# Kernel tuning notes

Hardware: AMD Instinct MI355X
Metric: run time of the kernel (lower is better)

The kernel has to match this reference:

```python
import jax, jax.numpy as jnp
import numpy as np

NUM_TAGS = 48
START = 46
STOP = 47
B = 1024
S = 512
NEG_INF = -10000.0


def setup_inputs() -> dict:
    key = jax.random.key(0)
    k1, k2, k3, k4 = jax.random.split(key, 4)
    emissions = jax.random.normal(k1, (B, S, NUM_TAGS), dtype=jnp.float32)
    tags = jax.random.randint(k2, (B, S), 0, 46, dtype=jnp.int32)
    lengths = jax.random.randint(k3, (B,), S // 2, S + 1, dtype=jnp.int32)
    mask = (jnp.arange(S, dtype=jnp.int32)[None, :] < lengths[:, None]).astype(jnp.int32)
    # transitions parameter: uniform(-0.1, 0.1), then constraints from reset_parameters
    transitions = jax.random.uniform(k4, (NUM_TAGS, NUM_TAGS), dtype=jnp.float32,
                                     minval=-0.1, maxval=0.1)
    transitions = transitions.at[:, START].set(NEG_INF).at[STOP, :].set(NEG_INF)
    return {"emissions": emissions, "tags": tags, "mask": mask, "transitions": transitions}


def _log_sum_exp(x, axis):
    # matches torch helper: max + log(clamp(sum(exp(x - max)), 1e-10))
    m = jnp.max(x, axis=axis, keepdims=True)
    s = jnp.sum(jnp.exp(x - m), axis=axis, keepdims=True)
    return jnp.squeeze(m + jnp.log(jnp.clip(s, 1e-10)), axis=axis)


def _forward_alg(emissions, transitions, mask):
    b, s, t = emissions.shape
    alpha0 = jnp.full((b, t), NEG_INF, dtype=emissions.dtype).at[:, START].set(0.0)

    def step(alpha, xs):
        emit, m = xs  # emit: (B, T), m: (B,)
        # (B, prev, next)
        nxt = alpha[:, :, None] + transitions[None, :, :] + emit[:, None, :]
        alpha_t = _log_sum_exp(nxt, axis=1)
        alpha = jnp.where(m[:, None] > 0, alpha_t, alpha)
        return alpha, None

    alpha, _ = jax.lax.scan(step, alpha0,
                            (jnp.transpose(emissions, (1, 0, 2)), mask.T))
    terminal = alpha + transitions[STOP][None, :]
    return _log_sum_exp(terminal, axis=1)  # (B,)


def _score_sequence(emissions, transitions, tags, mask):
    b, s, _ = emissions.shape
    start_col = jnp.full((b, 1), START, dtype=tags.dtype)
    tws = jnp.concatenate([start_col, tags], axis=1)  # (B, S+1)
    # transitions[next, prev] per the original _score_sequence
    trans_sc = transitions[tws[:, 1:], tws[:, :-1]]  # (B, S)
    emit_sc = jnp.take_along_axis(emissions, tags[:, :, None].astype(jnp.int32), axis=2)[..., 0]
    score = jnp.sum((trans_sc + emit_sc) * mask.astype(emissions.dtype), axis=1)
    lengths = jnp.sum(mask, axis=1)
    last_tags = jnp.take_along_axis(tags, (lengths - 1)[:, None], axis=1)[:, 0]
    return score + transitions[STOP, last_tags]


def reference(emissions, tags, mask, transitions):
    log_z = _forward_alg(emissions, transitions, mask)
    gold = _score_sequence(emissions, transitions, tags, mask)
    return jnp.mean(log_z - gold)
```

## Files before the change

kernel.cpp:

```cpp
#include <hip/hip_runtime.h>
#include <hip/hip_bf16.h>
#include <stdint.h>
#include <math.h>

#define SLEN 512
#define NT 48
#define TAG_START 46
#define TAG_STOP 47

typedef __attribute__((ext_vector_type(8))) short bf16x8;
typedef __attribute__((ext_vector_type(4))) float f32x4;

typedef const uint32_t __attribute__((address_space(1)))* gptr_t;
typedef uint32_t __attribute__((address_space(3)))* lptr_t;

__device__ __forceinline__ float bcastf(float v, int l) {
  return __int_as_float(__builtin_amdgcn_readlane(__float_as_int(v), l));
}
__device__ __forceinline__ void gload16(const float* g, float* l) {
  __builtin_amdgcn_global_load_lds((gptr_t)(uintptr_t)g, (lptr_t)(uintptr_t)l,
                                   16, 0, 0);
}
__device__ __forceinline__ uint32_t pk2(float a, float b) {
  float2 f;
  f.x = a;
  f.y = b;
  __hip_bfloat162 bb = __float22bfloat162_rn(f);
  uint32_t u;
  __builtin_memcpy(&u, &bb, 4);
  return u;
}

__global__ __launch_bounds__(64) void crf_fwd_kernel(
    const float* __restrict__ em, const int* __restrict__ tags,
    const int* __restrict__ mask, const float* __restrict__ Tr,
    float* __restrict__ ws) {
  const int b = blockIdx.x;
  const int lane = threadIdx.x;
  const int g = lane >> 4;
  const int n = lane & 15;
  __shared__ __align__(16) float lem[2][64 * NT];

  const int* mrow = mask + (size_t)b * SLEN;
  int lc = 0;
  for (int t = lane; t < SLEN; t += 64) lc += mrow[t];
#pragma unroll
  for (int d = 32; d >= 1; d >>= 1) lc += __shfl_xor(lc, d);
  const int len = lc;

  bf16x8 A[3][2];
#pragma unroll
  for (int t = 0; t < 3; ++t) {
#pragma unroll
    for (int c = 0; c < 2; ++c) {
      union { uint32_t u[4]; bf16x8 v; } tmp;
#pragma unroll
      for (int ep = 0; ep < 4; ++ep) {
        float fe[2];
#pragma unroll
        for (int h = 0; h < 2; ++h) {
          const int e = 2 * ep + h;
          const int kl = (e < 4) ? (4 * g + e) : (16 + 4 * g + (e - 4));
          const int ig = 32 * c + kl;
          fe[h] = (ig < NT) ? __expf(Tr[ig * NT + 16 * t + n]) : 0.0f;
        }
        tmp.u[ep] = pk2(fe[0], fe[1]);
      }
      A[t][c] = tmp.v;
    }
  }

  f32x4 v0 = {0.f, 0.f, 0.f, 0.f}, v1 = v0, v2 = v0;
  if (lane == 48) v2.z = 1.0f;
  int cbits = 0;

  const float* embase = em + (size_t)b * SLEN * NT;

  auto dostep = [&](const float* xb) {
    union { uint32_t u[4]; bf16x8 v; } B0, B1;
    B0.u[0] = pk2(v0.x, v0.y);
    B0.u[1] = pk2(v0.z, v0.w);
    B0.u[2] = pk2(v1.x, v1.y);
    B0.u[3] = pk2(v1.z, v1.w);
    B1.u[0] = pk2(v2.x, v2.y);
    B1.u[1] = pk2(v2.z, v2.w);
    B1.u[2] = 0u;
    B1.u[3] = 0u;
    const f32x4 z4 = {0.f, 0.f, 0.f, 0.f};
    f32x4 a0 = __builtin_amdgcn_mfma_f32_16x16x32_bf16(A[0][0], B0.v, z4, 0, 0, 0);
    f32x4 a1 = __builtin_amdgcn_mfma_f32_16x16x32_bf16(A[1][0], B0.v, z4, 0, 0, 0);
    f32x4 a2 = __builtin_amdgcn_mfma_f32_16x16x32_bf16(A[2][0], B0.v, z4, 0, 0, 0);
    a0 = __builtin_amdgcn_mfma_f32_16x16x32_bf16(A[0][1], B1.v, a0, 0, 0, 0);
    a1 = __builtin_amdgcn_mfma_f32_16x16x32_bf16(A[1][1], B1.v, a1, 0, 0, 0);
    a2 = __builtin_amdgcn_mfma_f32_16x16x32_bf16(A[2][1], B1.v, a2, 0, 0, 0);
    const f32x4 x0 = *(const f32x4*)(xb + 4 * g);
    const f32x4 x1 = *(const f32x4*)(xb + 16 + 4 * g);
    const f32x4 x2 = *(const f32x4*)(xb + 32 + 4 * g);
    v0 = a0 * x0;
    v1 = a1 * x1;
    v2 = a2 * x2;
  };

  auto renorm = [&]() {
    f32x4 m4 = __builtin_elementwise_max(__builtin_elementwise_max(v0, v1), v2);
    float m = fmaxf(fmaxf(m4.x, m4.y), fmaxf(m4.z, fmaxf(m4.w, 1e-30f)));
    m = fmaxf(fmaxf(bcastf(m, 0), bcastf(m, 16)),
              fmaxf(bcastf(m, 32), bcastf(m, 48)));
    int ex;
    (void)frexpf(m, &ex);
    const float sc = ldexpf(1.0f, -ex);
    v0 *= sc;
    v1 *= sc;
    v2 *= sc;
    cbits += ex;
  };

  const int nchunks = (len + 63) >> 6;
#pragma unroll
  for (int k = 0; k < 12; ++k)
    gload16(embase + k * 256 + lane * 4, &lem[0][k * 256]);

  for (int c = 0; c < nchunks; ++c) {
    asm volatile("s_waitcnt vmcnt(0)" ::: "memory");
    if (c + 1 < nchunks) {
      const float* src = embase + (size_t)(c + 1) * 64 * NT;
#pragma unroll
      for (int k = 0; k < 12; ++k)
        gload16(src + k * 256 + lane * 4, &lem[(c + 1) & 1][k * 256]);
    }
    float* bufm = lem[c & 1];
    {
      float* row = bufm + lane * NT;
#pragma unroll
      for (int r = 0; r < 12; ++r) {
        f32x4 vx = *(f32x4*)(row + 4 * r);
        vx.x = __expf(vx.x);
        vx.y = __expf(vx.y);
        vx.z = __expf(vx.z);
        vx.w = __expf(vx.w);
        *(f32x4*)(row + 4 * r) = vx;
      }
    }
    const int tend = (len - c * 64 < 64) ? (len - c * 64) : 64;
    int tt = 0;
    for (; tt + 8 <= tend; tt += 8) {
#pragma unroll
      for (int u2 = 0; u2 < 8; ++u2) dostep(bufm + (tt + u2) * NT);
      renorm();
    }
    for (; tt < tend; ++tt) dostep(bufm + tt * NT);
    renorm();
  }

  renorm();
  float zsum = (v0.x + v0.y + v0.z + v0.w) + (v1.x + v1.y + v1.z + v1.w) +
               (v2.x + v2.y + v2.z + v2.w);
#pragma unroll
  for (int d = 32; d >= 1; d >>= 1) zsum += __shfl_xor(zsum, d);
  const float logZ =
      __logf(zsum) + (float)cbits * 0.69314718055994531f + Tr[TAG_STOP * NT];

  const int* trow = tags + (size_t)b * SLEN;
  float gsc = 0.f;
  for (int t = lane; t < len; t += 64) {
    const int tag = trow[t];
    const int prev = (t == 0) ? TAG_START : trow[t - 1];
    gsc += Tr[tag * NT + prev] + embase[(size_t)t * NT + tag];
  }
#pragma unroll
  for (int d = 32; d >= 1; d >>= 1) gsc += __shfl_xor(gsc, d);

  if (lane == 0) {
    const int last = trow[len - 1];
    ws[b] = logZ - (gsc + Tr[TAG_STOP * NT + last]);
  }
}

__global__ void crf_reduce_kernel(const float* __restrict__ ws,
                                  float* __restrict__ out, int n) {
  const int tid = threadIdx.x;
  float v = (tid < n) ? ws[tid] : 0.f;
#pragma unroll
  for (int d = 32; d >= 1; d >>= 1) v += __shfl_xor(v, d);
  __shared__ float part[16];
  if ((tid & 63) == 0) part[tid >> 6] = v;
  __syncthreads();
  if (tid == 0) {
    float s = 0.f;
    for (int i = 0; i < 16; ++i) s += part[i];
    out[0] = s / (float)n;
  }
}

extern "C" void kernel_launch(void* const* d_in, const int* in_sizes, int n_in,
                              void* d_out, int out_size, void* d_ws, size_t ws_size,
                              hipStream_t stream) {
  const float* em = (const float*)d_in[0];
  const int* tags = (const int*)d_in[1];
  const int* mask = (const int*)d_in[2];
  const float* Tr = (const float*)d_in[3];
  const int B = in_sizes[0] / (SLEN * NT);

  float* ws = (float*)d_ws;
  crf_fwd_kernel<<<B, 64, 0, stream>>>(em, tags, mask, Tr, ws);
  crf_reduce_kernel<<<1, 1024, 0, stream>>>(ws, (float*)d_out, B);
}
```

Baseline: 97.33 us.

## Split CRF forward recursion into forward and backward halves meeting in the middle

Each sequence's linear-domain forward algorithm is split into a forward pass over the first half and a backward pass, using the transposed transition matrix, over the second half. Each block now handles two sequences in the two MFMA columns for one direction. A new combine kernel takes the dot product of the saved alpha and beta vectors to get logZ. This halves the serial dependency chain per block while keeping the same block count. It adds an extra kernel launch and workspace round-trip, and it also replaces the bf16 rounding pack with truncation and the renormalisation with cheaper bit tricks.

```diff
diff --git a/kernel.cpp b/kernel.cpp
--- a/kernel.cpp
+++ b/kernel.cpp
@@ -8,45 +8,63 @@
 #define TAG_START 46
 #define TAG_STOP 47
 
+#define WS_QF 0
+#define WS_WB 65536
+#define WS_OUT 131072
+
 typedef __attribute__((ext_vector_type(8))) short bf16x8;
 typedef __attribute__((ext_vector_type(4))) float f32x4;
 
 typedef const uint32_t __attribute__((address_space(1)))* gptr_t;
 typedef uint32_t __attribute__((address_space(3)))* lptr_t;
 
-__device__ __forceinline__ float bcastf(float v, int l) {
-  return __int_as_float(__builtin_amdgcn_readlane(__float_as_int(v), l));
-}
 __device__ __forceinline__ void gload16(const float* g, float* l) {
   __builtin_amdgcn_global_load_lds((gptr_t)(uintptr_t)g, (lptr_t)(uintptr_t)l,
                                    16, 0, 0);
 }
 __device__ __forceinline__ uint32_t pk2(float a, float b) {
-  float2 f;
-  f.x = a;
-  f.y = b;
-  __hip_bfloat162 bb = __float22bfloat162_rn(f);
-  uint32_t u;
-  __builtin_memcpy(&u, &bb, 4);
-  return u;
-}
-
-__global__ __launch_bounds__(64) void crf_fwd_kernel(
+  return __builtin_amdgcn_perm(__float_as_uint(b), __float_as_uint(a),
+                               0x07060302u);
+}
+__device__ __forceinline__ float fmax4(f32x4 v) {
+  return fmaxf(fmaxf(v.x, v.y), fmaxf(v.z, v.w));
+}
+
+__global__ __launch_bounds__(64) void crf_split2_kernel(
     const float* __restrict__ em, const int* __restrict__ tags,
     const int* __restrict__ mask, const float* __restrict__ Tr,
     float* __restrict__ ws) {
-  const int b = blockIdx.x;
+  const int bid = blockIdx.x;
+  const int dir = bid & 1;
+  const int p = bid >> 1;
+  const int b0 = 2 * p, b1 = 2 * p + 1;
   const int lane = threadIdx.x;
   const int g = lane >> 4;
   const int n = lane & 15;
-  __shared__ __align__(16) float lem[2][64 * NT];
-
-  const int* mrow = mask + (size_t)b * SLEN;
-  int lc = 0;
-  for (int t = lane; t < SLEN; t += 64) lc += mrow[t];
-#pragma unroll
-  for (int d = 32; d >= 1; d >>= 1) lc += __shfl_xor(lc, d);
-  const int len = lc;
+  __shared__ __align__(16) float sbuf[2][2][32 * NT];
+
+  int len0, len1;
+  {
+    int lc0 = 0, lc1 = 0;
+    const int* r0 = mask + (size_t)b0 * SLEN;
+    const int* r1 = mask + (size_t)b1 * SLEN;
+    for (int t = lane; t < SLEN; t += 64) {
+      lc0 += r0[t];
+      lc1 += r1[t];
+    }
+#pragma unroll
+    for (int d = 32; d >= 1; d >>= 1) {
+      lc0 += __shfl_xor(lc0, d);
+      lc1 += __shfl_xor(lc1, d);
+    }
+    len0 = lc0;
+    len1 = lc1;
+  }
+  const int m0 = len0 >> 1, m1 = len1 >> 1;
+  const int st0 = dir ? (len0 - m0) : m0;
+  const int st1 = dir ? (len1 - m1) : m1;
+  const int smax = (st0 > st1) ? st0 : st1;
+  const int my_st = (n == 0) ? st0 : ((n == 1) ? st1 : 0);
 
   bf16x8 A[3][2];
 #pragma unroll
@@ -62,7 +80,10 @@
           const int e = 2 * ep + h;
           const int kl = (e < 4) ? (4 * g + e) : (16 + 4 * g + (e - 4));
           const int ig = 32 * c + kl;
-          fe[h] = (ig < NT) ? __expf(Tr[ig * NT + 16 * t + n]) : 0.0f;
+          fe[h] = 0.0f;
+          if (ig < NT)
+            fe[h] = dir ? __expf(Tr[(16 * t + n) * NT + ig])
+                        : __expf(Tr[ig * NT + 16 * t + n]);
         }
         tmp.u[ep] = pk2(fe[0], fe[1]);
       }
@@ -70,116 +91,185 @@
     }
   }
 
-  f32x4 v0 = {0.f, 0.f, 0.f, 0.f}, v1 = v0, v2 = v0;
-  if (lane == 48) v2.z = 1.0f;
+  const f32x4 z4 = {0.f, 0.f, 0.f, 0.f};
+  f32x4 v0 = z4, v1 = z4, v2 = z4;
+  if (dir == 0) {
+    if (n < 2 && g == 3) v2.z = 1.0f;
+  } else {
+    if (n < 2) {
+      const f32x4 one4 = {1.f, 1.f, 1.f, 1.f};
+      v0 = one4;
+      v1 = one4;
+      v2 = one4;
+    }
+  }
   int cbits = 0;
-
-  const float* embase = em + (size_t)b * SLEN * NT;
-
-  auto dostep = [&](const float* xb) {
-    union { uint32_t u[4]; bf16x8 v; } B0, B1;
-    B0.u[0] = pk2(v0.x, v0.y);
-    B0.u[1] = pk2(v0.z, v0.w);
-    B0.u[2] = pk2(v1.x, v1.y);
-    B0.u[3] = pk2(v1.z, v1.w);
-    B1.u[0] = pk2(v2.x, v2.y);
-    B1.u[1] = pk2(v2.z, v2.w);
-    B1.u[2] = 0u;
-    B1.u[3] = 0u;
-    const f32x4 z4 = {0.f, 0.f, 0.f, 0.f};
-    f32x4 a0 = __builtin_amdgcn_mfma_f32_16x16x32_bf16(A[0][0], B0.v, z4, 0, 0, 0);
-    f32x4 a1 = __builtin_amdgcn_mfma_f32_16x16x32_bf16(A[1][0], B0.v, z4, 0, 0, 0);
-    f32x4 a2 = __builtin_amdgcn_mfma_f32_16x16x32_bf16(A[2][0], B0.v, z4, 0, 0, 0);
-    a0 = __builtin_amdgcn_mfma_f32_16x16x32_bf16(A[0][1], B1.v, a0, 0, 0, 0);
-    a1 = __builtin_amdgcn_mfma_f32_16x16x32_bf16(A[1][1], B1.v, a1, 0, 0, 0);
-    a2 = __builtin_amdgcn_mfma_f32_16x16x32_bf16(A[2][1], B1.v, a2, 0, 0, 0);
-    const f32x4 x0 = *(const f32x4*)(xb + 4 * g);
-    const f32x4 x1 = *(const f32x4*)(xb + 16 + 4 * g);
-    const f32x4 x2 = *(const f32x4*)(xb + 32 + 4 * g);
-    v0 = a0 * x0;
-    v1 = a1 * x1;
-    v2 = a2 * x2;
-  };
-
-  auto renorm = [&]() {
-    f32x4 m4 = __builtin_elementwise_max(__builtin_elementwise_max(v0, v1), v2);
-    float m = fmaxf(fmaxf(m4.x, m4.y), fmaxf(m4.z, fmaxf(m4.w, 1e-30f)));
-    m = fmaxf(fmaxf(bcastf(m, 0), bcastf(m, 16)),
-              fmaxf(bcastf(m, 32), bcastf(m, 48)));
-    int ex;
-    (void)frexpf(m, &ex);
-    const float sc = ldexpf(1.0f, -ex);
-    v0 *= sc;
-    v1 *= sc;
-    v2 *= sc;
-    cbits += ex;
-  };
-
-  const int nchunks = (len + 63) >> 6;
-#pragma unroll
-  for (int k = 0; k < 12; ++k)
-    gload16(embase + k * 256 + lane * 4, &lem[0][k * 256]);
-
-  for (int c = 0; c < nchunks; ++c) {
+  f32x4 sv0 = z4, sv1 = z4, sv2 = z4;
+  int scb = 0;
+
+  const float* eb0 = em + (size_t)b0 * SLEN * NT;
+  const float* eb1 = em + (size_t)b1 * SLEN * NT;
+  const int mybuf = (n == 1) ? 1 : 0;
+
+  const int nwin = (smax + 31) >> 5;
+
+  {
+    const float* s0 = dir ? (eb0 + (size_t)(len0 - 32) * NT) : eb0;
+    const float* s1 = dir ? (eb1 + (size_t)(len1 - 32) * NT) : eb1;
+#pragma unroll
+    for (int k = 0; k < 6; ++k) {
+      gload16(s0 + k * 256 + lane * 4, &sbuf[0][0][k * 256]);
+      gload16(s1 + k * 256 + lane * 4, &sbuf[0][1][k * 256]);
+    }
+  }
+
+  for (int c = 0; c < nwin; ++c) {
     asm volatile("s_waitcnt vmcnt(0)" ::: "memory");
-    if (c + 1 < nchunks) {
-      const float* src = embase + (size_t)(c + 1) * 64 * NT;
-#pragma unroll
-      for (int k = 0; k < 12; ++k)
-        gload16(src + k * 256 + lane * 4, &lem[(c + 1) & 1][k * 256]);
-    }
-    float* bufm = lem[c & 1];
+    if (c + 1 < nwin) {
+      const float* s0 = dir ? (eb0 + (size_t)(len0 - 32 * (c + 2)) * NT)
+                            : (eb0 + (size_t)(32 * (c + 1)) * NT);
+      const float* s1 = dir ? (eb1 + (size_t)(len1 - 32 * (c + 2)) * NT)
+                            : (eb1 + (size_t)(32 * (c + 1)) * NT);
+#pragma unroll
+      for (int k = 0; k < 6; ++k) {
+        gload16(s0 + k * 256 + lane * 4, &sbuf[(c + 1) & 1][0][k * 256]);
+        gload16(s1 + k * 256 + lane * 4, &sbuf[(c + 1) & 1][1][k * 256]);
+      }
+    }
     {
-      float* row = bufm + lane * NT;
+      float* base = &sbuf[c & 1][0][0];
 #pragma unroll
       for (int r = 0; r < 12; ++r) {
-        f32x4 vx = *(f32x4*)(row + 4 * r);
+        f32x4* pp = (f32x4*)(base + r * 256 + lane * 4);
+        f32x4 vx = *pp;
         vx.x = __expf(vx.x);
         vx.y = __expf(vx.y);
         vx.z = __expf(vx.z);
         vx.w = __expf(vx.w);
-        *(f32x4*)(row + 4 * r) = vx;
-      }
-    }
-    const int tend = (len - c * 64 < 64) ? (len - c * 64) : 64;
-    int tt = 0;
-    for (; tt + 8 <= tend; tt += 8) {
-#pragma unroll
-      for (int u2 = 0; u2 < 8; ++u2) dostep(bufm + (tt + u2) * NT);
-      renorm();
-    }
-    for (; tt < tend; ++tt) dostep(bufm + tt * NT);
-    renorm();
-  }
-
-  renorm();
-  float zsum = (v0.x + v0.y + v0.z + v0.w) + (v1.x + v1.y + v1.z + v1.w) +
-               (v2.x + v2.y + v2.z + v2.w);
-#pragma unroll
-  for (int d = 32; d >= 1; d >>= 1) zsum += __shfl_xor(zsum, d);
-  const float logZ =
-      __logf(zsum) + (float)cbits * 0.69314718055994531f + Tr[TAG_STOP * NT];
-
-  const int* trow = tags + (size_t)b * SLEN;
-  float gsc = 0.f;
-  for (int t = lane; t < len; t += 64) {
-    const int tag = trow[t];
-    const int prev = (t == 0) ? TAG_START : trow[t - 1];
-    gsc += Tr[tag * NT + prev] + embase[(size_t)t * NT + tag];
-  }
-#pragma unroll
-  for (int d = 32; d >= 1; d >>= 1) gsc += __shfl_xor(gsc, d);
-
+        *pp = vx;
+      }
+    }
+    const int steps = (smax - 32 * c < 32) ? (smax - 32 * c) : 32;
+    for (int sl = 0; sl < steps; ++sl) {
+      const int s = 32 * c + sl;
+      const int local = dir ? (31 - sl) : sl;
+      const float* xb = &sbuf[c & 1][mybuf][local * NT];
+      const f32x4 x0 = *(const f32x4*)(xb + 4 * g);
+      const f32x4 x1 = *(const f32x4*)(xb + 16 + 4 * g);
+      const f32x4 x2 = *(const f32x4*)(xb + 32 + 4 * g);
+      union { uint32_t u[4]; bf16x8 v; } B0, B1;
+      if (dir == 0) {
+        B0.u[0] = pk2(v0.x, v0.y);
+        B0.u[1] = pk2(v0.z, v0.w);
+        B0.u[2] = pk2(v1.x, v1.y);
+        B0.u[3] = pk2(v1.z, v1.w);
+        B1.u[0] = pk2(v2.x, v2.y);
+        B1.u[1] = pk2(v2.z, v2.w);
+        B1.u[2] = 0u;
+        B1.u[3] = 0u;
+      } else {
+        const f32x4 y0 = v0 * x0, y1 = v1 * x1, y2 = v2 * x2;
+        B0.u[0] = pk2(y0.x, y0.y);
+        B0.u[1] = pk2(y0.z, y0.w);
+        B0.u[2] = pk2(y1.x, y1.y);
+        B0.u[3] = pk2(y1.z, y1.w);
+        B1.u[0] = pk2(y2.x, y2.y);
+        B1.u[1] = pk2(y2.z, y2.w);
+        B1.u[2] = 0u;
+        B1.u[3] = 0u;
+      }
+      f32x4 a0 = __builtin_amdgcn_mfma_f32_16x16x32_bf16(A[0][0], B0.v, z4, 0, 0, 0);
+      f32x4 a1 = __builtin_amdgcn_mfma_f32_16x16x32_bf16(A[1][0], B0.v, z4, 0, 0, 0);
+      f32x4 a2 = __builtin_amdgcn_mfma_f32_16x16x32_bf16(A[2][0], B0.v, z4, 0, 0, 0);
+      a0 = __builtin_amdgcn_mfma_f32_16x16x32_bf16(A[0][1], B1.v, a0, 0, 0, 0);
+      a1 = __builtin_amdgcn_mfma_f32_16x16x32_bf16(A[1][1], B1.v, a1, 0, 0, 0);
+      a2 = __builtin_amdgcn_mfma_f32_16x16x32_bf16(A[2][1], B1.v, a2, 0, 0, 0);
+      if (dir == 0) {
+        v0 = a0 * x0;
+        v1 = a1 * x1;
+        v2 = a2 * x2;
+      } else {
+        v0 = a0;
+        v1 = a1;
+        v2 = a2;
+      }
+      if ((s & 7) == 7) {
+        float mx = fmaxf(fmax4(__builtin_elementwise_max(
+                             __builtin_elementwise_max(v0, v1), v2)),
+                         1e-30f);
+        mx = fmaxf(mx, __shfl_xor(mx, 16));
+        mx = fmaxf(mx, __shfl_xor(mx, 32));
+        const int ex = ((__float_as_int(mx) >> 23) & 255) - 126;
+        const float sc = __int_as_float((127 - ex) << 23);
+        v0 *= sc;
+        v1 *= sc;
+        v2 *= sc;
+        cbits += ex;
+      }
+      if (s + 1 == st0 || s + 1 == st1) {
+        const bool L = (n < 2) && (s + 1 == my_st);
+        sv0 = L ? v0 : sv0;
+        sv1 = L ? v1 : sv1;
+        sv2 = L ? v2 : sv2;
+        scb = L ? cbits : scb;
+      }
+    }
+  }
+
+  if (n < 2) {
+    const int bb = n ? b1 : b0;
+    float* dst = ws + (dir ? WS_WB : WS_QF) + (size_t)bb * 64;
+    *(f32x4*)(dst + 4 * g) = sv0;
+    *(f32x4*)(dst + 16 + 4 * g) = sv1;
+    *(f32x4*)(dst + 32 + 4 * g) = sv2;
+    if (g == 0) dst[48] = (float)scb;
+  }
+
+  if (dir == 0) {
+#pragma unroll
+    for (int which = 0; which < 2; ++which) {
+      const int bb = which ? b1 : b0;
+      const int ll = which ? len1 : len0;
+      const float* eb = which ? eb1 : eb0;
+      const int* trow = tags + (size_t)bb * SLEN;
+      float gsc = 0.f;
+      for (int t = lane; t < ll; t += 64) {
+        const int tag = trow[t];
+        const int prev = (t == 0) ? TAG_START : trow[t - 1];
+        gsc += Tr[tag * NT + prev] + eb[(size_t)t * NT + tag];
+      }
+#pragma unroll
+      for (int d = 32; d >= 1; d >>= 1) gsc += __shfl_xor(gsc, d);
+      if (lane == 0) {
+        const int last = trow[ll - 1];
+        ws[WS_QF + (size_t)bb * 64 + 49] = gsc + Tr[TAG_STOP * NT + last];
+      }
+    }
+  }
+}
+
+__global__ __launch_bounds__(64) void crf_combine_kernel(
+    const float* __restrict__ Tr, float* __restrict__ ws) {
+  const int b = blockIdx.x;
+  const int lane = threadIdx.x;
+  float p = 0.f;
+  if (lane < NT)
+    p = ws[WS_QF + (size_t)b * 64 + lane] * ws[WS_WB + (size_t)b * 64 + lane];
+#pragma unroll
+  for (int d = 32; d >= 1; d >>= 1) p += __shfl_xor(p, d);
   if (lane == 0) {
-    const int last = trow[len - 1];
-    ws[b] = logZ - (gsc + Tr[TAG_STOP * NT + last]);
-  }
-}
-
-__global__ void crf_reduce_kernel(const float* __restrict__ ws,
-                                  float* __restrict__ out, int n) {
+    const float cb =
+        ws[WS_QF + (size_t)b * 64 + 48] + ws[WS_WB + (size_t)b * 64 + 48];
+    const float gold = ws[WS_QF + (size_t)b * 64 + 49];
+    ws[WS_OUT + b] =
+        __logf(p) + cb * 0.69314718055994531f + Tr[TAG_STOP * NT] - gold;
+  }
+}
+
+__global__ void crf_reduce_kernel(const float* __restrict__ wsrc,
+                                  float* __restrict__ out, int nn) {
   const int tid = threadIdx.x;
-  float v = (tid < n) ? ws[tid] : 0.f;
+  float v = (tid < nn) ? wsrc[tid] : 0.f;
 #pragma unroll
   for (int d = 32; d >= 1; d >>= 1) v += __shfl_xor(v, d);
   __shared__ float part[16];
@@ -188,7 +278,7 @@
   if (tid == 0) {
     float s = 0.f;
     for (int i = 0; i < 16; ++i) s += part[i];
-    out[0] = s / (float)n;
+    out[0] = s / (float)nn;
   }
 }
 
@@ -202,6 +292,7 @@
   const int B = in_sizes[0] / (SLEN * NT);
 
   float* ws = (float*)d_ws;
-  crf_fwd_kernel<<<B, 64, 0, stream>>>(em, tags, mask, Tr, ws);
-  crf_reduce_kernel<<<1, 1024, 0, stream>>>(ws, (float*)d_out, B);
-}
+  crf_split2_kernel<<<B, 64, 0, stream>>>(em, tags, mask, Tr, ws);
+  crf_combine_kernel<<<B, 64, 0, stream>>>(Tr, ws);
+  crf_reduce_kernel<<<1, 1024, 0, stream>>>(ws + WS_OUT, (float*)d_out, B);
+}
```

New measurement: 94.23 us. 3.2% less time.
